# Performance work log

Hardware: AMD Instinct MI355X
Metric: run time of the kernel (lower is better)

The kernel has to match this reference:

```python
import jax, jax.numpy as jnp
import numpy as np

B, T, D, H, R = 4, 4096, 1024, 16, 256
DH = D // H  # 64


def setup_inputs() -> dict:
    key = jax.random.key(0)
    ks = jax.random.split(key, 5)
    s = 0.02
    return {
        "x": jax.random.normal(ks[0], (B, T, D), dtype=jnp.float32),
        "Wq": jax.random.normal(ks[1], (D, D), dtype=jnp.float32) * s,
        "bq": jnp.zeros((D,), dtype=jnp.float32),
        "Wd": jax.random.normal(ks[2], (D, R), dtype=jnp.float32) * s,
        "bd": jnp.zeros((R,), dtype=jnp.float32),
        "Wu": jax.random.normal(ks[3], (R, 2 * D), dtype=jnp.float32) * s,
        "bu": jnp.zeros((2 * D,), dtype=jnp.float32),
        "Wo": jax.random.normal(ks[4], (D, D), dtype=jnp.float32) * s,
        "bo": jnp.zeros((D,), dtype=jnp.float32),
    }


def reference(x, Wq, bq, Wd, bd, Wu, bu, Wo, bo):
    b, t = x.shape[0], x.shape[1]
    # q projection -> (B,T,H,DH)
    q = (x @ Wq + bq).reshape(b, t, H, DH)
    # low-rank KV: down then up -> (B,T,H,2*DH)
    kv = ((x @ Wd + bd) @ Wu + bu).reshape(b, t, H, 2 * DH)
    k, v = kv[..., :DH], kv[..., DH:]
    # elu+1 feature map
    q = jax.nn.elu(q) + 1.0
    k = jax.nn.elu(k) + 1.0
    # linear attention: context = k^T v per head -> (B,H,DH,DH)
    context = jnp.einsum("bthd,bthe->bhde", k, v)
    out = jnp.einsum("bthd,bhde->bthe", q, context)  # (B,T,H,DH)
    # normalizer: q . sum_t(k)
    k_sum = k.sum(axis=1)  # (B,H,DH)
    z = 1.0 / (jnp.einsum("bthd,bhd->bth", q, k_sum) + 1e-6)
    out = out * z[..., None]
    return out.reshape(b, t, D) @ Wo + bo
```

## Files before the change

kernel.cpp:

```cpp
#include <hip/hip_runtime.h>
#include <hip/hip_bf16.h>
#include <cstddef>
#include <cstdint>

#define B_  4
#define T_  4096
#define D_  1024
#define H_  16
#define DH_ 64
#define R_  256
#define BT_ (B_ * T_)
#define TWO_D_ (2 * D_)

typedef __attribute__((ext_vector_type(8))) short short8;
typedef __attribute__((ext_vector_type(4))) float f32x4;

__device__ __forceinline__ float elu1(float x) {
    return x > 0.0f ? x + 1.0f : __expf(x);
}

__device__ __forceinline__ float bf2f(short u) {
    union { uint32_t i; float f; } c;
    c.i = ((uint32_t)(uint16_t)u) << 16;
    return c.f;
}

typedef __attribute__((address_space(1))) void void_g;
typedef __attribute__((address_space(3))) void void_l;
__device__ __forceinline__ void gld_lds16(const void* g, void* l) {
    __builtin_amdgcn_global_load_lds(
        (const void_g*)(uintptr_t)g,
        (void_l*)(uint32_t)(uintptr_t)l,
        16, 0, 0);
}

__device__ __forceinline__ void store_out(float* p, float v) { *p = v; }
__device__ __forceinline__ void store_out(__hip_bfloat16* p, float v) { *p = __float2bfloat16(v); }

#define PBM 256
#define PBN 256

template<int EPI, bool BROW, typename OT>
__global__ __launch_bounds__(512, 2) void gemm_p8(
    const __hip_bfloat16* __restrict__ A,
    const __hip_bfloat16* __restrict__ Bt,
    const float* __restrict__ bias,
    OT* __restrict__ C,
    int M, int N, int K)
{
    __shared__ alignas(16) __hip_bfloat16 sm[65536];
    __hip_bfloat16* Asm = sm;
    __hip_bfloat16* Bsm = sm + 32768;

    const int nbx = N / PBN;
    const int nbm = M / PBM;
    const int sh = (nbm < 8) ? nbm : 8;
    const int id = blockIdx.x;
    const int wi = id % (sh * nbx);
    const int bm = ((id / (sh * nbx)) * sh + (wi % sh)) * PBM;
    const int bn = (wi / sh) * PBN;

    const int tid  = threadIdx.x;
    const int lane = tid & 63;
    const int w    = tid >> 6;
    const int wm   = w >> 2;
    const int wn   = w & 3;
    const int r15  = lane & 15;
    const int kg   = lane >> 4;

    const int nt = K / 64;

    const int rl = tid >> 3;
    const int g  = (tid & 7) ^ (rl & 7);
    const __hip_bfloat16* aS = A  + (size_t)(bm + rl) * K + g * 8;
    const __hip_bfloat16* bS = Bt + (size_t)(bn + rl) * K + g * 8;
    __hip_bfloat16* dA = Asm + tid * 8;
    __hip_bfloat16* dB = Bsm + tid * 8;

    auto stA = [&](int t, int h) {
        const int tc = (t < nt) ? t : (nt - 1);
        __hip_bfloat16* d = dA + ((t & 1) * 2 + h) * 8192;
        const __hip_bfloat16* s = aS + (size_t)(h * 128) * K + tc * 64;
        gld_lds16(s, d);
        gld_lds16(s + (size_t)64 * K, d + 4096);
    };
    auto stB = [&](int t, int h) {
        const int tc = (t < nt) ? t : (nt - 1);
        __hip_bfloat16* d = dB + ((t & 1) * 2 + h) * 8192;
        const __hip_bfloat16* s = bS + (size_t)(h * 128) * K + tc * 64;
        gld_lds16(s, d);
        gld_lds16(s + (size_t)64 * K, d + 4096);
    };

    const int x3    = (r15 & 7) << 3;
    const int kofs0 = (kg * 8) ^ x3;
    const int kofs1 = (32 + kg * 8) ^ x3;
    const __hip_bfloat16* Af0 = Asm + wm * 8192 + r15 * 64;
    const __hip_bfloat16* Bf0 = Bsm + (wn >> 1) * 8192 + (wn & 1) * 4096 + r15 * 64;
    const __hip_bfloat16* Af1 = Af0 + 16384;
    const __hip_bfloat16* Bf1 = Bf0 + 16384;

    f32x4 acc[8][4] = {};
    short8 af[8][2], bf[4][2];

    stA(0, 0); stA(0, 1); stB(0, 0); stB(0, 1); stA(1, 0); stA(1, 1);
    asm volatile("s_waitcnt vmcnt(4)" ::: "memory");
    __builtin_amdgcn_s_barrier();

    for (int t = 0; t < nt; t += 2) {
#pragma unroll
        for (int i = 0; i < 4; ++i) {
            af[i][0] = *(const short8*)(Af0 + i * 1024 + kofs0);
            af[i][1] = *(const short8*)(Af0 + i * 1024 + kofs1);
        }
#pragma unroll
        for (int j = 0; j < 2; ++j) {
            bf[j][0] = *(const short8*)(Bf0 + j * 1024 + kofs0);
            bf[j][1] = *(const short8*)(Bf0 + j * 1024 + kofs1);
        }
        stB(t + 1, 0);
        __builtin_amdgcn_s_barrier();
        asm volatile("s_waitcnt lgkmcnt(0)" ::: "memory");
        __builtin_amdgcn_sched_barrier(0);
        __builtin_amdgcn_s_setprio(1);
#pragma unroll
        for (int i = 0; i < 4; ++i)
#pragma unroll
            for (int j = 0; j < 2; ++j) {
                acc[i][j] = __builtin_amdgcn_mfma_f32_16x16x32_bf16(af[i][0], bf[j][0], acc[i][j], 0, 0, 0);
                acc[i][j] = __builtin_amdgcn_mfma_f32_16x16x32_bf16(af[i][1], bf[j][1], acc[i][j], 0, 0, 0);
            }
        __builtin_amdgcn_s_setprio(0);
        __builtin_amdgcn_s_barrier();

#pragma unroll
        for (int i = 4; i < 8; ++i) {
            af[i][0] = *(const short8*)(Af0 + i * 1024 + kofs0);
            af[i][1] = *(const short8*)(Af0 + i * 1024 + kofs1);
        }
        stB(t + 1, 1);
        __builtin_amdgcn_s_barrier();
        asm volatile("s_waitcnt lgkmcnt(0)" ::: "memory");
        __builtin_amdgcn_sched_barrier(0);
        __builtin_amdgcn_s_setprio(1);
#pragma unroll
        for (int i = 4; i < 8; ++i)
#pragma unroll
            for (int j = 0; j < 2; ++j) {
                acc[i][j] = __builtin_amdgcn_mfma_f32_16x16x32_bf16(af[i][0], bf[j][0], acc[i][j], 0, 0, 0);
                acc[i][j] = __builtin_amdgcn_mfma_f32_16x16x32_bf16(af[i][1], bf[j][1], acc[i][j], 0, 0, 0);
            }
        __builtin_amdgcn_s_setprio(0);
        __builtin_amdgcn_s_barrier();

#pragma unroll
        for (int j = 2; j < 4; ++j) {
            bf[j][0] = *(const short8*)(Bf0 + j * 1024 + kofs0);
            bf[j][1] = *(const short8*)(Bf0 + j * 1024 + kofs1);
        }
        stA(t + 2, 0);
        __builtin_amdgcn_s_barrier();
        asm volatile("s_waitcnt lgkmcnt(0)" ::: "memory");
        __builtin_amdgcn_sched_barrier(0);
        __builtin_amdgcn_s_setprio(1);
#pragma unroll
        for (int i = 4; i < 8; ++i)
#pragma unroll
            for (int j = 2; j < 4; ++j) {
                acc[i][j] = __builtin_amdgcn_mfma_f32_16x16x32_bf16(af[i][0], bf[j][0], acc[i][j], 0, 0, 0);
                acc[i][j] = __builtin_amdgcn_mfma_f32_16x16x32_bf16(af[i][1], bf[j][1], acc[i][j], 0, 0, 0);
            }
        __builtin_amdgcn_s_setprio(0);
        __builtin_amdgcn_s_barrier();

        stA(t + 2, 1);
        asm volatile("s_waitcnt vmcnt(4)" ::: "memory");
        __builtin_amdgcn_s_barrier();
        __builtin_amdgcn_sched_barrier(0);
        __builtin_amdgcn_s_setprio(1);
#pragma unroll
        for (int i = 0; i < 4; ++i)
#pragma unroll
            for (int j = 2; j < 4; ++j) {
                acc[i][j] = __builtin_amdgcn_mfma_f32_16x16x32_bf16(af[i][0], bf[j][0], acc[i][j], 0, 0, 0);
                acc[i][j] = __builtin_amdgcn_mfma_f32_16x16x32_bf16(af[i][1], bf[j][1], acc[i][j], 0, 0, 0);
            }
        __builtin_amdgcn_s_setprio(0);
        __builtin_amdgcn_s_barrier();

#pragma unroll
        for (int i = 0; i < 4; ++i) {
            af[i][0] = *(const short8*)(Af1 + i * 1024 + kofs0);
            af[i][1] = *(const short8*)(Af1 + i * 1024 + kofs1);
        }
#pragma unroll
        for (int j = 0; j < 2; ++j) {
            bf[j][0] = *(const short8*)(Bf1 + j * 1024 + kofs0);
            bf[j][1] = *(const short8*)(Bf1 + j * 1024 + kofs1);
        }
        stB(t + 2, 0);
        __builtin_amdgcn_s_barrier();
        asm volatile("s_waitcnt lgkmcnt(0)" ::: "memory");
        __builtin_amdgcn_sched_barrier(0);
        __builtin_amdgcn_s_setprio(1);
#pragma unroll
        for (int i = 0; i < 4; ++i)
#pragma unroll
            for (int j = 0; j < 2; ++j) {
                acc[i][j] = __builtin_amdgcn_mfma_f32_16x16x32_bf16(af[i][0], bf[j][0], acc[i][j], 0, 0, 0);
                acc[i][j] = __builtin_amdgcn_mfma_f32_16x16x32_bf16(af[i][1], bf[j][1], acc[i][j], 0, 0, 0);
            }
        __builtin_amdgcn_s_setprio(0);
        __builtin_amdgcn_s_barrier();

#pragma unroll
        for (int i = 4; i < 8; ++i) {
            af[i][0] = *(const short8*)(Af1 + i * 1024 + kofs0);
            af[i][1] = *(const short8*)(Af1 + i * 1024 + kofs1);
        }
        stB(t + 2, 1);
        __builtin_amdgcn_s_barrier();
        asm volatile("s_waitcnt lgkmcnt(0)" ::: "memory");
        __builtin_amdgcn_sched_barrier(0);
        __builtin_amdgcn_s_setprio(1);
#pragma unroll
        for (int i = 4; i < 8; ++i)
#pragma unroll
            for (int j = 0; j < 2; ++j) {
                acc[i][j] = __builtin_amdgcn_mfma_f32_16x16x32_bf16(af[i][0], bf[j][0], acc[i][j], 0, 0, 0);
                acc[i][j] = __builtin_amdgcn_mfma_f32_16x16x32_bf16(af[i][1], bf[j][1], acc[i][j], 0, 0, 0);
            }
        __builtin_amdgcn_s_setprio(0);
        __builtin_amdgcn_s_barrier();

#pragma unroll
        for (int j = 2; j < 4; ++j) {
            bf[j][0] = *(const short8*)(Bf1 + j * 1024 + kofs0);
            bf[j][1] = *(const short8*)(Bf1 + j * 1024 + kofs1);
        }
        stA(t + 3, 0);
        __builtin_amdgcn_s_barrier();
        asm volatile("s_waitcnt lgkmcnt(0)" ::: "memory");
        __builtin_amdgcn_sched_barrier(0);
        __builtin_amdgcn_s_setprio(1);
#pragma unroll
        for (int i = 4; i < 8; ++i)
#pragma unroll
            for (int j = 2; j < 4; ++j) {
                acc[i][j] = __builtin_amdgcn_mfma_f32_16x16x32_bf16(af[i][0], bf[j][0], acc[i][j], 0, 0, 0);
                acc[i][j] = __builtin_amdgcn_mfma_f32_16x16x32_bf16(af[i][1], bf[j][1], acc[i][j], 0, 0, 0);
            }
        __builtin_amdgcn_s_setprio(0);
        __builtin_amdgcn_s_barrier();

        stA(t + 3, 1);
        asm volatile("s_waitcnt vmcnt(4)" ::: "memory");
        __builtin_amdgcn_s_barrier();
        __builtin_amdgcn_sched_barrier(0);
        __builtin_amdgcn_s_setprio(1);
#pragma unroll
        for (int i = 0; i < 4; ++i)
#pragma unroll
            for (int j = 2; j < 4; ++j) {
                acc[i][j] = __builtin_amdgcn_mfma_f32_16x16x32_bf16(af[i][0], bf[j][0], acc[i][j], 0, 0, 0);
                acc[i][j] = __builtin_amdgcn_mfma_f32_16x16x32_bf16(af[i][1], bf[j][1], acc[i][j], 0, 0, 0);
            }
        __builtin_amdgcn_s_setprio(0);
        __builtin_amdgcn_s_barrier();
    }
    asm volatile("s_waitcnt vmcnt(0)" ::: "memory");

    const int row0 = bm + wm * 128 + (lane >> 4) * 4;

    float brow[8][4];
    if (BROW) {
#pragma unroll
        for (int i = 0; i < 8; ++i)
#pragma unroll
            for (int r = 0; r < 4; ++r) brow[i][r] = bias[row0 + i * 16 + r];
    }
#pragma unroll
    for (int j = 0; j < 4; ++j) {
        const int col = bn + wn * 64 + j * 16 + r15;
        const float bv = BROW ? 0.0f : bias[col];
        const bool kp_col = ((col & 127) < 64);
#pragma unroll
        for (int i = 0; i < 8; ++i) {
#pragma unroll
            for (int r = 0; r < 4; ++r) {
                const int row = row0 + i * 16 + r;
                float v = acc[i][j][r] + (BROW ? brow[i][r] : bv);
                if (EPI == 1) v = elu1(v);
                else if (EPI == 2) {
                    const bool kp = BROW ? ((row & 127) < 64) : kp_col;
                    if (kp) v = elu1(v);
                }
                store_out(C + (size_t)row * N + col, v);
            }
        }
    }
}

#define BM 128
#define BN 128
#define BK 32
#define NBUF 5

template<int EPI, bool BROW, typename OT>
__global__ __launch_bounds__(256) void gemm_bf16(
    const __hip_bfloat16* __restrict__ A,
    const __hip_bfloat16* __restrict__ Bt,
    const float* __restrict__ bias,
    OT* __restrict__ C,
    OT* __restrict__ C2,
    int M, int N, int K)
{
    __shared__ alignas(16) __hip_bfloat16 As[NBUF * BM * BK];
    __shared__ alignas(16) __hip_bfloat16 Bs[NBUF * BN * BK];

    const int nbx = N / BN;
    const int id = blockIdx.x;
    const int strip = id / (8 * nbx);
    const int wi = id % (8 * nbx);
    const int bm = (strip * 8 + (wi & 7)) * BM;
    const int bn = (wi >> 3) * BN;

    const int tid  = threadIdx.x;
    const int lane = tid & 63;
    const int wm   = (tid >> 7) * 64;
    const int wn   = ((tid >> 6) & 1) * 64;
    const int r15  = lane & 15;
    const int kg   = lane >> 4;

    f32x4 acc[4][4] = {};

    const int c0 = tid, c1 = tid + 256;
    const __hip_bfloat16* a0 = A  + (size_t)(bm + (c0 >> 2)) * K + (c0 & 3) * 8;
    const __hip_bfloat16* a1 = A  + (size_t)(bm + (c1 >> 2)) * K + (c1 & 3) * 8;
    const __hip_bfloat16* b0 = Bt + (size_t)(bn + (c0 >> 2)) * K + (c0 & 3) * 8;
    const __hip_bfloat16* b1 = Bt + (size_t)(bn + (c1 >> 2)) * K + (c1 & 3) * 8;

    const int nk = K / BK;

    auto stage = [&](int t) {
        const int buf = t % NBUF;
        __hip_bfloat16* Ad = As + buf * (BM * BK);
        __hip_bfloat16* Bd = Bs + buf * (BN * BK);
        const int k0 = t * BK;
        gld_lds16(a0 + k0, Ad + c0 * 8);
        gld_lds16(a1 + k0, Ad + c1 * 8);
        gld_lds16(b0 + k0, Bd + c0 * 8);
        gld_lds16(b1 + k0, Bd + c1 * 8);
    };

    stage(0); stage(1); stage(2);

    for (int t = 0; t < nk; ++t) {
        if (t + 3 < nk) {
            stage(t + 3);
            asm volatile("s_waitcnt vmcnt(12)\ns_barrier" ::: "memory");
        } else if (t + 2 < nk) {
            asm volatile("s_waitcnt vmcnt(8)\ns_barrier" ::: "memory");
        } else if (t + 1 < nk) {
            asm volatile("s_waitcnt vmcnt(4)\ns_barrier" ::: "memory");
        } else {
            asm volatile("s_waitcnt vmcnt(0)\ns_barrier" ::: "memory");
        }

        const __hip_bfloat16* Asb = As + (t % NBUF) * (BM * BK);
        const __hip_bfloat16* Bsb = Bs + (t % NBUF) * (BN * BK);

        short8 af[4], bf[4];
#pragma unroll
        for (int i = 0; i < 4; ++i) {
            af[i] = *(const short8*)(Asb + (wm + i * 16 + r15) * BK + kg * 8);
            bf[i] = *(const short8*)(Bsb + (wn + i * 16 + r15) * BK + kg * 8);
        }
#pragma unroll
        for (int i = 0; i < 4; ++i)
#pragma unroll
            for (int j = 0; j < 4; ++j)
                acc[i][j] = __builtin_amdgcn_mfma_f32_16x16x32_bf16(af[i], bf[j], acc[i][j], 0, 0, 0);
    }

    const int row0 = bm + wm + (lane >> 4) * 4;

    if (EPI == 3) {
        const bool qreg = (bn < 1024);
#pragma unroll
        for (int j = 0; j < 4; ++j) {
            const int col = bn + wn + j * 16 + r15;
            const float bv = bias[col];
#pragma unroll
            for (int i = 0; i < 4; ++i)
#pragma unroll
                for (int r = 0; r < 4; ++r) {
                    const int row = row0 + i * 16 + r;
                    float v = acc[i][j][r] + bv;
                    if (qreg) {
                        store_out(C + (size_t)row * 1024 + col, elu1(v));
                    } else {
                        store_out(C2 + (size_t)row * 256 + (col - 1024), v);
                    }
                }
        }
        return;
    }

    float brow[4][4];
    if (BROW) {
#pragma unroll
        for (int i = 0; i < 4; ++i)
#pragma unroll
            for (int r = 0; r < 4; ++r) brow[i][r] = bias[row0 + i * 16 + r];
    }
#pragma unroll
    for (int j = 0; j < 4; ++j) {
        const int col = bn + wn + j * 16 + r15;
        const float bv = BROW ? 0.0f : bias[col];
        const bool kp_col = ((col & 127) < 64);
#pragma unroll
        for (int i = 0; i < 4; ++i) {
#pragma unroll
            for (int r = 0; r < 4; ++r) {
                const int row = row0 + i * 16 + r;
                float v = acc[i][j][r] + (BROW ? brow[i][r] : bv);
                if (EPI == 1) v = elu1(v);
                else if (EPI == 2) {
                    const bool kp = BROW ? ((row & 127) < 64) : kp_col;
                    if (kp) v = elu1(v);
                }
                store_out(C + (size_t)row * N + col, v);
            }
        }
    }
}

__global__ __launch_bounds__(256) void cast_bf16_kernel(
    const float* __restrict__ s, __hip_bfloat16* __restrict__ d, int n)
{
    const int i = (blockIdx.x * 256 + threadIdx.x) * 8;
    if (i >= n) return;
    float4 v0 = *(const float4*)(s + i);
    float4 v1 = *(const float4*)(s + i + 4);
    __hip_bfloat16 t[8];
    t[0] = __float2bfloat16(v0.x); t[1] = __float2bfloat16(v0.y);
    t[2] = __float2bfloat16(v0.z); t[3] = __float2bfloat16(v0.w);
    t[4] = __float2bfloat16(v1.x); t[5] = __float2bfloat16(v1.y);
    t[6] = __float2bfloat16(v1.z); t[7] = __float2bfloat16(v1.w);
    *(short8*)(d + i) = *(const short8*)t;
}

__global__ __launch_bounds__(256) void transpose_cast(
    const float* __restrict__ W, __hip_bfloat16* __restrict__ Wt, int K, int N)
{
    __shared__ float t[32][33];
    const int n0 = blockIdx.x * 32, k0 = blockIdx.y * 32;
    const int c = threadIdx.x & 31, r = threadIdx.x >> 5;
#pragma unroll
    for (int rr = r; rr < 32; rr += 8)
        t[rr][c] = W[(size_t)(k0 + rr) * N + n0 + c];
    __syncthreads();
#pragma unroll
    for (int rr = r; rr < 32; rr += 8)
        Wt[(size_t)(n0 + rr) * K + k0 + c] = __float2bfloat16(t[c][rr]);
}

#define CHT 512

__global__ __launch_bounds__(256) void ctx_mfma(
    const __hip_bfloat16* __restrict__ kvT, float* __restrict__ ctx,
    float* __restrict__ ksum)
{
    __shared__ alignas(16) unsigned char smem[40960];
    float* red0 = (float*)smem;
    float* red1 = (float*)(smem + 20480);

    const int bh = blockIdx.x >> 3;
    const int chunk = blockIdx.x & 7;
    const int b = bh >> 4;
    const int h = bh & 15;
    const int tid = threadIdx.x;
    const int lane = tid & 63;
    const int w = tid >> 6;
    const int r15 = lane & 15;
    const int kg  = lane >> 4;

    f32x4 acc[4][4] = {};
    f32x4 acc4[4] = {};

    const short one = (short)0x3F80;
    const short8 bfv = (r15 == 0)
        ? (short8){one, one, one, one, one, one, one, one}
        : (short8){0, 0, 0, 0, 0, 0, 0, 0};

    const size_t tbase = (size_t)b * T_ + (size_t)chunk * CHT;
    const __hip_bfloat16* src = kvT + (size_t)(h * 128) * BT_ + tbase;

    for (int it = 0; it < CHT / 128; ++it) {
#pragma unroll
        for (int r = 0; r < 8; ++r) {
            const int c = r * 256 + tid;
            const int s = c >> 9, j = (c >> 2) & 127, u = c & 3;
            gld_lds16(src + (size_t)j * BT_ + it * 128 + s * 32 + u * 8,
                      smem + c * 16);
        }
        __syncthreads();

        const __hip_bfloat16* Ls = (const __hip_bfloat16*)smem;
        short8 af[4], bf[4];
#pragma unroll
        for (int i = 0; i < 4; ++i) {
            af[i] = *(const short8*)(Ls + (w * 128 + i * 16 + r15) * 32 + kg * 8);
            bf[i] = *(const short8*)(Ls + (w * 128 + 64 + i * 16 + r15) * 32 + kg * 8);
        }
#pragma unroll
        for (int i = 0; i < 4; ++i) {
#pragma unroll
            for (int j = 0; j < 4; ++j)
                acc[i][j] = __builtin_amdgcn_mfma_f32_16x16x32_bf16(af[i], bf[j], acc[i][j], 0, 0, 0);
            acc4[i] = __builtin_amdgcn_mfma_f32_16x16x32_bf16(af[i], bfv, acc4[i], 0, 0, 0);
        }
        __syncthreads();
    }

    const int q4 = lane >> 4;
    auto wr = [&](float* reg) {
#pragma unroll
        for (int i = 0; i < 4; ++i) {
#pragma unroll
            for (int r = 0; r < 4; ++r) {
                const int row = i * 16 + q4 * 4 + r;
#pragma unroll
                for (int j = 0; j < 4; ++j) reg[row * 80 + j * 16 + r15] = acc[i][j][r];
                reg[row * 80 + 64 + r15] = acc4[i][r];
            }
        }
    };
    auto rd = [&](const float* reg) {
#pragma unroll
        for (int i = 0; i < 4; ++i) {
#pragma unroll
            for (int r = 0; r < 4; ++r) {
                const int row = i * 16 + q4 * 4 + r;
#pragma unroll
                for (int j = 0; j < 4; ++j) acc[i][j][r] += reg[row * 80 + j * 16 + r15];
                acc4[i][r] += reg[row * 80 + 64 + r15];
            }
        }
    };

    if (w == 1) wr(red0);
    if (w == 3) wr(red1);
    __syncthreads();
    if (w == 0) rd(red0);
    if (w == 2) rd(red1);
    __syncthreads();
    if (w == 2) wr(red0);
    __syncthreads();
    if (w == 0) { rd(red0); wr(red0); }
    __syncthreads();

    float* cdst = ctx + (size_t)bh * 4096;
#pragma unroll
    for (int r = 0; r < 16; ++r) {
        const int idx = r * 256 + tid;
        const int d = idx >> 6, e = idx & 63;
        atomicAdd(cdst + idx, red0[d * 80 + e]);
    }
    if (tid < 64) atomicAdd(ksum + bh * 64 + tid, red0[tid * 80 + 64]);
}

__global__ __launch_bounds__(256) void pack_ctx(
    const float* __restrict__ ctx, __hip_bfloat16* __restrict__ ctxT)
{
    __shared__ float L[64 * 65];
    const int bh = blockIdx.x;
    const int tid = threadIdx.x;
#pragma unroll
    for (int r = 0; r < 16; ++r) {
        const int idx = r * 256 + tid;
        L[(idx >> 6) * 65 + (idx & 63)] = ctx[(size_t)bh * 4096 + idx];
    }
    __syncthreads();
#pragma unroll
    for (int r = 0; r < 16; ++r) {
        const int idx = r * 256 + tid;
        ctxT[(size_t)bh * 4096 + idx] =
            __float2bfloat16(L[(idx & 63) * 65 + (idx >> 6)]);
    }
}

__global__ __launch_bounds__(256) void out_mfma(
    const __hip_bfloat16* __restrict__ qb, const __hip_bfloat16* __restrict__ ctxT,
    const float* __restrict__ ksum, __hip_bfloat16* __restrict__ outb)
{
    __shared__ alignas(16) unsigned char As[256 * 128];
    __shared__ alignas(16) unsigned char Bs[64 * 128];
    __shared__ float ksumL[64];
    __shared__ float zbuf[256];

    const int bh = blockIdx.x >> 4;
    const int tile = blockIdx.x & 15;
    const int b = bh >> 4;
    const int h = bh & 15;
    const int tid = threadIdx.x;
    const int lane = tid & 63;
    const int w = tid >> 6;
    const int r15 = lane & 15;
    const int kg  = lane >> 4;

    const size_t trow0 = (size_t)b * T_ + (size_t)tile * 256;

#pragma unroll
    for (int r = 0; r < 8; ++r) {
        const int c = r * 256 + tid;
        const int row = c >> 3, slot = c & 7, u = slot ^ (row & 7);
        gld_lds16(qb + (trow0 + row) * D_ + h * 64 + u * 8, As + c * 16);
    }
#pragma unroll
    for (int r = 0; r < 2; ++r) {
        const int c = r * 256 + tid;
        const int row = c >> 3, slot = c & 7, u = slot ^ (row & 7);
        gld_lds16(ctxT + (size_t)bh * 4096 + row * 64 + u * 8, Bs + c * 16);
    }
    if (tid < 64) ksumL[tid] = ksum[bh * 64 + tid];
    __syncthreads();

    short8 af[4][2], bf[4][2];
#pragma unroll
    for (int i = 0; i < 4; ++i)
#pragma unroll
        for (int s = 0; s < 2; ++s) {
            const int m = w * 64 + i * 16 + r15;
            const int n = i * 16 + r15;
            const int uk = s * 4 + kg;
            af[i][s] = *(const short8*)(As + m * 128 + ((uk ^ (m & 7)) * 16));
            bf[i][s] = *(const short8*)(Bs + n * 128 + ((uk ^ (n & 7)) * 16));
        }

    f32x4 acc[4][4] = {};
#pragma unroll
    for (int s = 0; s < 2; ++s)
#pragma unroll
        for (int i = 0; i < 4; ++i)
#pragma unroll
            for (int j = 0; j < 4; ++j)
                acc[i][j] = __builtin_amdgcn_mfma_f32_16x16x32_bf16(af[i][s], bf[j][s], acc[i][j], 0, 0, 0);

    float dsum[4];
#pragma unroll
    for (int i = 0; i < 4; ++i) {
        float s0 = 0.0f;
#pragma unroll
        for (int s = 0; s < 2; ++s)
#pragma unroll
            for (int j8 = 0; j8 < 8; ++j8)
                s0 += bf2f(af[i][s][j8]) * ksumL[s * 32 + kg * 8 + j8];
        s0 += __shfl_xor(s0, 16);
        s0 += __shfl_xor(s0, 32);
        dsum[i] = s0;
    }
    if (lane < 16) {
#pragma unroll
        for (int i = 0; i < 4; ++i)
            zbuf[w * 64 + i * 16 + lane] = 1.0f / (dsum[i] + 1e-6f);
    }
    __syncthreads();

    const int q4 = lane >> 4;
#pragma unroll
    for (int i = 0; i < 4; ++i) {
#pragma unroll
        for (int r = 0; r < 4; ++r) {
            const int m = w * 64 + i * 16 + q4 * 4 + r;
            const float z = zbuf[m];
#pragma unroll
            for (int j = 0; j < 4; ++j) {
                outb[(trow0 + m) * D_ + h * 64 + j * 16 + r15] =
                    __float2bfloat16(acc[i][j][r] * z);
            }
        }
    }
}

extern "C" void kernel_launch(void* const* d_in, const int* in_sizes, int n_in,
                              void* d_out, int out_size, void* d_ws, size_t ws_size,
                              hipStream_t stream) {
    const float* x  = (const float*)d_in[0];
    const float* Wq = (const float*)d_in[1];
    const float* bq = (const float*)d_in[2];
    const float* Wd = (const float*)d_in[3];
    const float* bd = (const float*)d_in[4];
    const float* Wu = (const float*)d_in[5];
    const float* bu = (const float*)d_in[6];
    const float* Wo = (const float*)d_in[7];
    const float* bo = (const float*)d_in[8];
    float* out = (float*)d_out;

    __hip_bfloat16* xb    = (__hip_bfloat16*)d_ws;
    __hip_bfloat16* WqdT  = xb    + (size_t)BT_ * D_;
    __hip_bfloat16* WuT   = WqdT  + (size_t)1280 * D_;
    __hip_bfloat16* WoT   = WuT   + (size_t)TWO_D_ * R_;
    __hip_bfloat16* xdb   = WoT   + (size_t)D_ * D_;
    __hip_bfloat16* kvT   = xdb   + (size_t)BT_ * R_;
    __hip_bfloat16* qb    = kvT   + (size_t)TWO_D_ * BT_;
    float* bias_qd = (float*)(qb + (size_t)BT_ * D_);
    float* ctx  = bias_qd + 1280;
    float* ksum = ctx + (size_t)B_ * H_ * DH_ * DH_;
    __hip_bfloat16* ctxT = (__hip_bfloat16*)(ksum + B_ * H_ * DH_);
    __hip_bfloat16* outb = xb;

    hipMemsetAsync(ctx, 0,
        (size_t)(B_ * H_ * DH_ * DH_ + B_ * H_ * DH_) * sizeof(float), stream);

    cast_bf16_kernel<<<(BT_ * D_) / (8 * 256), 256, 0, stream>>>(x, xb, BT_ * D_);
    transpose_cast<<<dim3(D_ / 32, D_ / 32), 256, 0, stream>>>(Wq, WqdT, D_, D_);
    transpose_cast<<<dim3(R_ / 32, D_ / 32), 256, 0, stream>>>(Wd, WqdT + (size_t)D_ * D_, D_, R_);
    transpose_cast<<<dim3(TWO_D_ / 32, R_ / 32), 256, 0, stream>>>(Wu, WuT, R_, TWO_D_);
    transpose_cast<<<dim3(D_ / 32, D_ / 32), 256, 0, stream>>>(Wo, WoT, D_, D_);

    gemm_bf16<0, false, __hip_bfloat16><<<(BT_ / BM) * (R_ / BN), 256, 0, stream>>>(
        xb, WqdT + (size_t)D_ * D_, bd, xdb, nullptr, BT_, R_, D_);
    gemm_p8<1, false, __hip_bfloat16><<<(BT_ / PBM) * (D_ / PBN), 512, 0, stream>>>(
        xb, WqdT, bq, qb, BT_, D_, D_);
    gemm_p8<2, true, __hip_bfloat16><<<(TWO_D_ / PBM) * (BT_ / PBN), 512, 0, stream>>>(
        WuT, xdb, bu, kvT, TWO_D_, BT_, R_);
    ctx_mfma<<<64 * (T_ / CHT), 256, 0, stream>>>(kvT, ctx, ksum);
    pack_ctx<<<64, 256, 0, stream>>>(ctx, ctxT);
    out_mfma<<<64 * 16, 256, 0, stream>>>(qb, ctxT, ksum, outb);
    gemm_p8<0, false, float><<<(BT_ / PBM) * (D_ / PBN), 512, 0, stream>>>(
        outb, WoT, bo, out, BT_, D_, D_);
}
```

Measured before the change: 326.5 us.

## Split LDS fragment waits per k-half in GEMM and fuse prep kernels

The main GEMM loop now issues the LDS fragment reads in two k-halves and waits only for the first half before starting MFMAs, so the second half's reads overlap compute. Separately, the input cast, the four weight transpose-casts and the context zeroing memset are merged into a single prep kernel dispatched by block index. This removes several launches and the memset. The finer-grained waitcnt values depend on exact instruction ordering, which the sched barriers enforce.

```diff
diff --git a/kernel.cpp b/kernel.cpp
--- a/kernel.cpp
+++ b/kernel.cpp
@@ -103,172 +103,157 @@
     f32x4 acc[8][4] = {};
     short8 af[8][2], bf[4][2];
 
+#define RDA(i, ks, BASE) af[i][ks] = *(const short8*)((BASE) + (i) * 1024 + ((ks) ? kofs1 : kofs0))
+#define RDB(j, ks, BASE) bf[j][ks] = *(const short8*)((BASE) + (j) * 1024 + ((ks) ? kofs1 : kofs0))
+#define MM(ILO, IHI, JLO, JHI, KS)                                             \
+    _Pragma("unroll")                                                          \
+    for (int i = (ILO); i < (IHI); ++i)                                        \
+        _Pragma("unroll")                                                      \
+        for (int j = (JLO); j < (JHI); ++j)                                    \
+            acc[i][j] = __builtin_amdgcn_mfma_f32_16x16x32_bf16(af[i][KS], bf[j][KS], acc[i][j], 0, 0, 0)
+#define SB0() __builtin_amdgcn_sched_barrier(0)
+
     stA(0, 0); stA(0, 1); stB(0, 0); stB(0, 1); stA(1, 0); stA(1, 1);
     asm volatile("s_waitcnt vmcnt(4)" ::: "memory");
     __builtin_amdgcn_s_barrier();
 
     for (int t = 0; t < nt; t += 2) {
 #pragma unroll
-        for (int i = 0; i < 4; ++i) {
-            af[i][0] = *(const short8*)(Af0 + i * 1024 + kofs0);
-            af[i][1] = *(const short8*)(Af0 + i * 1024 + kofs1);
-        }
-#pragma unroll
-        for (int j = 0; j < 2; ++j) {
-            bf[j][0] = *(const short8*)(Bf0 + j * 1024 + kofs0);
-            bf[j][1] = *(const short8*)(Bf0 + j * 1024 + kofs1);
-        }
+        for (int i = 0; i < 4; ++i) RDA(i, 0, Af0);
+#pragma unroll
+        for (int j = 0; j < 2; ++j) RDB(j, 0, Bf0);
+        SB0();
+#pragma unroll
+        for (int i = 0; i < 4; ++i) RDA(i, 1, Af0);
+#pragma unroll
+        for (int j = 0; j < 2; ++j) RDB(j, 1, Bf0);
         stB(t + 1, 0);
         __builtin_amdgcn_s_barrier();
+        asm volatile("s_waitcnt lgkmcnt(6)" ::: "memory");
+        SB0();
+        __builtin_amdgcn_s_setprio(1);
+        MM(0, 4, 0, 2, 0);
         asm volatile("s_waitcnt lgkmcnt(0)" ::: "memory");
-        __builtin_amdgcn_sched_barrier(0);
+        SB0();
+        MM(0, 4, 0, 2, 1);
+        __builtin_amdgcn_s_setprio(0);
+        __builtin_amdgcn_s_barrier();
+
+#pragma unroll
+        for (int i = 4; i < 8; ++i) RDA(i, 0, Af0);
+        SB0();
+#pragma unroll
+        for (int i = 4; i < 8; ++i) RDA(i, 1, Af0);
+        stB(t + 1, 1);
+        __builtin_amdgcn_s_barrier();
+        asm volatile("s_waitcnt lgkmcnt(4)" ::: "memory");
+        SB0();
         __builtin_amdgcn_s_setprio(1);
-#pragma unroll
-        for (int i = 0; i < 4; ++i)
-#pragma unroll
-            for (int j = 0; j < 2; ++j) {
-                acc[i][j] = __builtin_amdgcn_mfma_f32_16x16x32_bf16(af[i][0], bf[j][0], acc[i][j], 0, 0, 0);
-                acc[i][j] = __builtin_amdgcn_mfma_f32_16x16x32_bf16(af[i][1], bf[j][1], acc[i][j], 0, 0, 0);
-            }
+        MM(4, 8, 0, 2, 0);
+        asm volatile("s_waitcnt lgkmcnt(0)" ::: "memory");
+        SB0();
+        MM(4, 8, 0, 2, 1);
         __builtin_amdgcn_s_setprio(0);
         __builtin_amdgcn_s_barrier();
 
 #pragma unroll
-        for (int i = 4; i < 8; ++i) {
-            af[i][0] = *(const short8*)(Af0 + i * 1024 + kofs0);
-            af[i][1] = *(const short8*)(Af0 + i * 1024 + kofs1);
-        }
-        stB(t + 1, 1);
-        __builtin_amdgcn_s_barrier();
+        for (int j = 2; j < 4; ++j) RDB(j, 0, Bf0);
+        SB0();
+#pragma unroll
+        for (int j = 2; j < 4; ++j) RDB(j, 1, Bf0);
+        stA(t + 2, 0);
+        __builtin_amdgcn_s_barrier();
+        asm volatile("s_waitcnt lgkmcnt(2)" ::: "memory");
+        SB0();
+        __builtin_amdgcn_s_setprio(1);
+        MM(4, 8, 2, 4, 0);
         asm volatile("s_waitcnt lgkmcnt(0)" ::: "memory");
-        __builtin_amdgcn_sched_barrier(0);
-        __builtin_amdgcn_s_setprio(1);
-#pragma unroll
-        for (int i = 4; i < 8; ++i)
-#pragma unroll
-            for (int j = 0; j < 2; ++j) {
-                acc[i][j] = __builtin_amdgcn_mfma_f32_16x16x32_bf16(af[i][0], bf[j][0], acc[i][j], 0, 0, 0);
-                acc[i][j] = __builtin_amdgcn_mfma_f32_16x16x32_bf16(af[i][1], bf[j][1], acc[i][j], 0, 0, 0);
-            }
-        __builtin_amdgcn_s_setprio(0);
-        __builtin_amdgcn_s_barrier();
-
-#pragma unroll
-        for (int j = 2; j < 4; ++j) {
-            bf[j][0] = *(const short8*)(Bf0 + j * 1024 + kofs0);
-            bf[j][1] = *(const short8*)(Bf0 + j * 1024 + kofs1);
-        }
-        stA(t + 2, 0);
-        __builtin_amdgcn_s_barrier();
-        asm volatile("s_waitcnt lgkmcnt(0)" ::: "memory");
-        __builtin_amdgcn_sched_barrier(0);
-        __builtin_amdgcn_s_setprio(1);
-#pragma unroll
-        for (int i = 4; i < 8; ++i)
-#pragma unroll
-            for (int j = 2; j < 4; ++j) {
-                acc[i][j] = __builtin_amdgcn_mfma_f32_16x16x32_bf16(af[i][0], bf[j][0], acc[i][j], 0, 0, 0);
-                acc[i][j] = __builtin_amdgcn_mfma_f32_16x16x32_bf16(af[i][1], bf[j][1], acc[i][j], 0, 0, 0);
-            }
+        SB0();
+        MM(4, 8, 2, 4, 1);
         __builtin_amdgcn_s_setprio(0);
         __builtin_amdgcn_s_barrier();
 
         stA(t + 2, 1);
         asm volatile("s_waitcnt vmcnt(4)" ::: "memory");
         __builtin_amdgcn_s_barrier();
-        __builtin_amdgcn_sched_barrier(0);
+        SB0();
         __builtin_amdgcn_s_setprio(1);
-#pragma unroll
-        for (int i = 0; i < 4; ++i)
-#pragma unroll
-            for (int j = 2; j < 4; ++j) {
-                acc[i][j] = __builtin_amdgcn_mfma_f32_16x16x32_bf16(af[i][0], bf[j][0], acc[i][j], 0, 0, 0);
-                acc[i][j] = __builtin_amdgcn_mfma_f32_16x16x32_bf16(af[i][1], bf[j][1], acc[i][j], 0, 0, 0);
-            }
+        MM(0, 4, 2, 4, 0);
+        MM(0, 4, 2, 4, 1);
         __builtin_amdgcn_s_setprio(0);
         __builtin_amdgcn_s_barrier();
 
 #pragma unroll
-        for (int i = 0; i < 4; ++i) {
-            af[i][0] = *(const short8*)(Af1 + i * 1024 + kofs0);
-            af[i][1] = *(const short8*)(Af1 + i * 1024 + kofs1);
-        }
-#pragma unroll
-        for (int j = 0; j < 2; ++j) {
-            bf[j][0] = *(const short8*)(Bf1 + j * 1024 + kofs0);
-            bf[j][1] = *(const short8*)(Bf1 + j * 1024 + kofs1);
-        }
+        for (int i = 0; i < 4; ++i) RDA(i, 0, Af1);
+#pragma unroll
+        for (int j = 0; j < 2; ++j) RDB(j, 0, Bf1);
+        SB0();
+#pragma unroll
+        for (int i = 0; i < 4; ++i) RDA(i, 1, Af1);
+#pragma unroll
+        for (int j = 0; j < 2; ++j) RDB(j, 1, Bf1);
         stB(t + 2, 0);
         __builtin_amdgcn_s_barrier();
+        asm volatile("s_waitcnt lgkmcnt(6)" ::: "memory");
+        SB0();
+        __builtin_amdgcn_s_setprio(1);
+        MM(0, 4, 0, 2, 0);
         asm volatile("s_waitcnt lgkmcnt(0)" ::: "memory");
-        __builtin_amdgcn_sched_barrier(0);
+        SB0();
+        MM(0, 4, 0, 2, 1);
+        __builtin_amdgcn_s_setprio(0);
+        __builtin_amdgcn_s_barrier();
+
+#pragma unroll
+        for (int i = 4; i < 8; ++i) RDA(i, 0, Af1);
+        SB0();
+#pragma unroll
+        for (int i = 4; i < 8; ++i) RDA(i, 1, Af1);
+        stB(t + 2, 1);
+        __builtin_amdgcn_s_barrier();
+        asm volatile("s_waitcnt lgkmcnt(4)" ::: "memory");
+        SB0();
         __builtin_amdgcn_s_setprio(1);
-#pragma unroll
-        for (int i = 0; i < 4; ++i)
-#pragma unroll
-            for (int j = 0; j < 2; ++j) {
-                acc[i][j] = __builtin_amdgcn_mfma_f32_16x16x32_bf16(af[i][0], bf[j][0], acc[i][j], 0, 0, 0);
-                acc[i][j] = __builtin_amdgcn_mfma_f32_16x16x32_bf16(af[i][1], bf[j][1], acc[i][j], 0, 0, 0);
-            }
+        MM(4, 8, 0, 2, 0);
+        asm volatile("s_waitcnt lgkmcnt(0)" ::: "memory");
+        SB0();
+        MM(4, 8, 0, 2, 1);
         __builtin_amdgcn_s_setprio(0);
         __builtin_amdgcn_s_barrier();
 
 #pragma unroll
-        for (int i = 4; i < 8; ++i) {
-            af[i][0] = *(const short8*)(Af1 + i * 1024 + kofs0);
-            af[i][1] = *(const short8*)(Af1 + i * 1024 + kofs1);
-        }
-        stB(t + 2, 1);
-        __builtin_amdgcn_s_barrier();
+        for (int j = 2; j < 4; ++j) RDB(j, 0, Bf1);
+        SB0();
+#pragma unroll
+        for (int j = 2; j < 4; ++j) RDB(j, 1, Bf1);
+        stA(t + 3, 0);
+        __builtin_amdgcn_s_barrier();
+        asm volatile("s_waitcnt lgkmcnt(2)" ::: "memory");
+        SB0();
+        __builtin_amdgcn_s_setprio(1);
+        MM(4, 8, 2, 4, 0);
         asm volatile("s_waitcnt lgkmcnt(0)" ::: "memory");
-        __builtin_amdgcn_sched_barrier(0);
-        __builtin_amdgcn_s_setprio(1);
-#pragma unroll
-        for (int i = 4; i < 8; ++i)
-#pragma unroll
-            for (int j = 0; j < 2; ++j) {
-                acc[i][j] = __builtin_amdgcn_mfma_f32_16x16x32_bf16(af[i][0], bf[j][0], acc[i][j], 0, 0, 0);
-                acc[i][j] = __builtin_amdgcn_mfma_f32_16x16x32_bf16(af[i][1], bf[j][1], acc[i][j], 0, 0, 0);
-            }
-        __builtin_amdgcn_s_setprio(0);
-        __builtin_amdgcn_s_barrier();
-
-#pragma unroll
-        for (int j = 2; j < 4; ++j) {
-            bf[j][0] = *(const short8*)(Bf1 + j * 1024 + kofs0);
-            bf[j][1] = *(const short8*)(Bf1 + j * 1024 + kofs1);
-        }
-        stA(t + 3, 0);
-        __builtin_amdgcn_s_barrier();
-        asm volatile("s_waitcnt lgkmcnt(0)" ::: "memory");
-        __builtin_amdgcn_sched_barrier(0);
-        __builtin_amdgcn_s_setprio(1);
-#pragma unroll
-        for (int i = 4; i < 8; ++i)
-#pragma unroll
-            for (int j = 2; j < 4; ++j) {
-                acc[i][j] = __builtin_amdgcn_mfma_f32_16x16x32_bf16(af[i][0], bf[j][0], acc[i][j], 0, 0, 0);
-                acc[i][j] = __builtin_amdgcn_mfma_f32_16x16x32_bf16(af[i][1], bf[j][1], acc[i][j], 0, 0, 0);
-            }
+        SB0();
+        MM(4, 8, 2, 4, 1);
         __builtin_amdgcn_s_setprio(0);
         __builtin_amdgcn_s_barrier();
 
         stA(t + 3, 1);
         asm volatile("s_waitcnt vmcnt(4)" ::: "memory");
         __builtin_amdgcn_s_barrier();
-        __builtin_amdgcn_sched_barrier(0);
+        SB0();
         __builtin_amdgcn_s_setprio(1);
-#pragma unroll
-        for (int i = 0; i < 4; ++i)
-#pragma unroll
-            for (int j = 2; j < 4; ++j) {
-                acc[i][j] = __builtin_amdgcn_mfma_f32_16x16x32_bf16(af[i][0], bf[j][0], acc[i][j], 0, 0, 0);
-                acc[i][j] = __builtin_amdgcn_mfma_f32_16x16x32_bf16(af[i][1], bf[j][1], acc[i][j], 0, 0, 0);
-            }
+        MM(0, 4, 2, 4, 0);
+        MM(0, 4, 2, 4, 1);
         __builtin_amdgcn_s_setprio(0);
         __builtin_amdgcn_s_barrier();
     }
     asm volatile("s_waitcnt vmcnt(0)" ::: "memory");
+
+#undef RDA
+#undef RDB
+#undef MM
+#undef SB0
 
     const int row0 = bm + wm * 128 + (lane >> 4) * 4;
 
@@ -436,27 +421,12 @@
     }
 }
 
-__global__ __launch_bounds__(256) void cast_bf16_kernel(
-    const float* __restrict__ s, __hip_bfloat16* __restrict__ d, int n)
+__device__ __forceinline__ void tcast_body(
+    const float* __restrict__ W, __hip_bfloat16* __restrict__ Wt,
+    int K, int N, int bx, int by, int tid, float (*t)[33])
 {
-    const int i = (blockIdx.x * 256 + threadIdx.x) * 8;
-    if (i >= n) return;
-    float4 v0 = *(const float4*)(s + i);
-    float4 v1 = *(const float4*)(s + i + 4);
-    __hip_bfloat16 t[8];
-    t[0] = __float2bfloat16(v0.x); t[1] = __float2bfloat16(v0.y);
-    t[2] = __float2bfloat16(v0.z); t[3] = __float2bfloat16(v0.w);
-    t[4] = __float2bfloat16(v1.x); t[5] = __float2bfloat16(v1.y);
-    t[6] = __float2bfloat16(v1.z); t[7] = __float2bfloat16(v1.w);
-    *(short8*)(d + i) = *(const short8*)t;
-}
-
-__global__ __launch_bounds__(256) void transpose_cast(
-    const float* __restrict__ W, __hip_bfloat16* __restrict__ Wt, int K, int N)
-{
-    __shared__ float t[32][33];
-    const int n0 = blockIdx.x * 32, k0 = blockIdx.y * 32;
-    const int c = threadIdx.x & 31, r = threadIdx.x >> 5;
+    const int n0 = bx * 32, k0 = by * 32;
+    const int c = tid & 31, r = tid >> 5;
 #pragma unroll
     for (int rr = r; rr < 32; rr += 8)
         t[rr][c] = W[(size_t)(k0 + rr) * N + n0 + c];
@@ -464,6 +434,50 @@
 #pragma unroll
     for (int rr = r; rr < 32; rr += 8)
         Wt[(size_t)(n0 + rr) * K + k0 + c] = __float2bfloat16(t[c][rr]);
+}
+
+__global__ __launch_bounds__(256) void prep(
+    const float* __restrict__ x,
+    const float* __restrict__ Wq, const float* __restrict__ Wd,
+    const float* __restrict__ Wu, const float* __restrict__ Wo,
+    __hip_bfloat16* __restrict__ xb,
+    __hip_bfloat16* __restrict__ WqdT, __hip_bfloat16* __restrict__ WuT,
+    __hip_bfloat16* __restrict__ WoT,
+    float* __restrict__ zbase)
+{
+    __shared__ float t[32][33];
+    const int id = blockIdx.x;
+    const int tid = threadIdx.x;
+
+    if (id < 8192) {
+        const int i = (id * 256 + tid) * 8;
+        float4 v0 = *(const float4*)(x + i);
+        float4 v1 = *(const float4*)(x + i + 4);
+        __hip_bfloat16 tt[8];
+        tt[0] = __float2bfloat16(v0.x); tt[1] = __float2bfloat16(v0.y);
+        tt[2] = __float2bfloat16(v0.z); tt[3] = __float2bfloat16(v0.w);
+        tt[4] = __float2bfloat16(v1.x); tt[5] = __float2bfloat16(v1.y);
+        tt[6] = __float2bfloat16(v1.z); tt[7] = __float2bfloat16(v1.w);
+        *(short8*)(xb + i) = *(const short8*)tt;
+    } else if (id < 8192 + 1024) {
+        const int u = id - 8192;
+        tcast_body(Wq, WqdT, D_, D_, u & 31, u >> 5, tid, t);
+    } else if (id < 8192 + 1280) {
+        const int u = id - (8192 + 1024);
+        tcast_body(Wd, WqdT + (size_t)D_ * D_, D_, R_, u & 7, u >> 3, tid, t);
+    } else if (id < 8192 + 1792) {
+        const int u = id - (8192 + 1280);
+        tcast_body(Wu, WuT, R_, TWO_D_, u & 63, u >> 6, tid, t);
+    } else if (id < 8192 + 2816) {
+        const int u = id - (8192 + 1792);
+        tcast_body(Wo, WoT, D_, D_, u & 31, u >> 5, tid, t);
+    } else {
+        const int u = id - (8192 + 2816);
+        const int i = (u * 256 + tid) * 8;
+        float4 z = {0.f, 0.f, 0.f, 0.f};
+        *(float4*)(zbase + i) = z;
+        *(float4*)(zbase + i + 4) = z;
+    }
 }
 
 #define CHT 512
@@ -711,14 +725,8 @@
     __hip_bfloat16* ctxT = (__hip_bfloat16*)(ksum + B_ * H_ * DH_);
     __hip_bfloat16* outb = xb;
 
-    hipMemsetAsync(ctx, 0,
-        (size_t)(B_ * H_ * DH_ * DH_ + B_ * H_ * DH_) * sizeof(float), stream);
-
-    cast_bf16_kernel<<<(BT_ * D_) / (8 * 256), 256, 0, stream>>>(x, xb, BT_ * D_);
-    transpose_cast<<<dim3(D_ / 32, D_ / 32), 256, 0, stream>>>(Wq, WqdT, D_, D_);
-    transpose_cast<<<dim3(R_ / 32, D_ / 32), 256, 0, stream>>>(Wd, WqdT + (size_t)D_ * D_, D_, R_);
-    transpose_cast<<<dim3(TWO_D_ / 32, R_ / 32), 256, 0, stream>>>(Wu, WuT, R_, TWO_D_);
-    transpose_cast<<<dim3(D_ / 32, D_ / 32), 256, 0, stream>>>(Wo, WoT, D_, D_);
+    prep<<<8192 + 2816 + 130, 256, 0, stream>>>(
+        x, Wq, Wd, Wu, Wo, xb, WqdT, WuT, WoT, ctx);
 
     gemm_bf16<0, false, __hip_bfloat16><<<(BT_ / BM) * (R_ / BN), 256, 0, stream>>>(
         xb, WqdT + (size_t)D_ * D_, bd, xdb, nullptr, BT_, R_, D_);
```

After: 311.8 us. 1.05x faster.
